# Kernel tuning notes

Hardware: AMD Instinct MI355X
Metric: run time of the kernel (lower is better)

Reference implementation:

```python
import jax, jax.numpy as jnp
import numpy as np

DIM = 3072
NHEADS = 24
HEAD_DIM = DIM // NHEADS  # 128
C = HEAD_DIM // 2         # 64 rotary pairs
B = 2
L = 2048
MAXPOS = 64
EPS = 1e-6
C1 = C - 2 * (C // 3)     # 22 (F band)
C2 = C // 3               # 21 (H band)
C3 = C // 3               # 21 (W band)


def _rope_table():
    # cos/sin table [MAXPOS, C, 2]; three independent frequency bands (F,H,W)
    pos = np.arange(MAXPOS, dtype=np.float32)
    parts = []
    for ck in (C1, C2, C3):
        inv = 1.0 / (10000.0 ** (np.arange(ck, dtype=np.float32) / ck))
        ang = np.outer(pos, inv)
        parts.append(np.stack([np.cos(ang), np.sin(ang)], axis=-1))
    return np.concatenate(parts, axis=1).astype(np.float32)


def setup_inputs() -> dict:
    key = jax.random.key(0)
    ks = jax.random.split(key, 12)
    x = jax.random.normal(ks[0], (B, L, DIM), dtype=jnp.float32)
    grid_sizes = np.array([[4, 16, 28], [4, 16, 32]], dtype=np.int32)  # ragged: 1792, 2048 tokens
    seq_lens = np.array([g[0] * g[1] * g[2] for g in grid_sizes], dtype=np.int32)
    freqs = jnp.asarray(_rope_table())
    w_scale = 0.02
    wq = jax.random.normal(ks[1], (DIM, DIM), dtype=jnp.float32) * w_scale
    wk = jax.random.normal(ks[2], (DIM, DIM), dtype=jnp.float32) * w_scale
    wv = jax.random.normal(ks[3], (DIM, DIM), dtype=jnp.float32) * w_scale
    wo = jax.random.normal(ks[4], (DIM, DIM), dtype=jnp.float32) * w_scale
    bq = jnp.zeros((DIM,), jnp.float32)
    bk = jnp.zeros((DIM,), jnp.float32)
    bv = jnp.zeros((DIM,), jnp.float32)
    bo = jnp.zeros((DIM,), jnp.float32)
    gq = jnp.ones((DIM,), jnp.float32)  # norm_q weight
    gk = jnp.ones((DIM,), jnp.float32)  # norm_k weight
    return {"x": x, "seq_lens": seq_lens, "grid_sizes": grid_sizes, "freqs": freqs,
            "wq": wq, "bq": bq, "wk": wk, "bk": bk, "wv": wv, "bv": bv,
            "wo": wo, "bo": bo, "gq": gq, "gk": gk}


def _rmsnorm(x, g):
    # WanRMSNorm: normalize in bf16, cast back, scale by bf16 weight
    xb = x.astype(jnp.bfloat16)
    n = xb * jax.lax.rsqrt(jnp.mean(xb * xb, axis=-1, keepdims=True) + jnp.bfloat16(EPS))
    return n.astype(x.dtype) * g.astype(jnp.bfloat16)


def _build_rot(grid_sizes, freqs):
    # Per-sample 3D rope rotation table [B, L, C, 2]; padded tail gets identity rotation
    gs = np.asarray(grid_sizes)
    rots = []
    for f, h, w in gs.tolist():
        s = f * h * w
        bf = jnp.broadcast_to(freqs[:f, :C1][:, None, None], (f, h, w, C1, 2))
        bh = jnp.broadcast_to(freqs[:h, C1:C1 + C2][None, :, None], (f, h, w, C2, 2))
        bw = jnp.broadcast_to(freqs[:w, C1 + C2:][None, None, :], (f, h, w, C3, 2))
        rot = jnp.concatenate([bf, bh, bw], axis=3).reshape(s, C, 2)
        if s < L:
            ident = jnp.zeros((L - s, C, 2), freqs.dtype).at[..., 0].set(1.0)
            rot = jnp.concatenate([rot, ident], axis=0)
        rots.append(rot)
    return jnp.stack(rots)


def _apply_rope(x, rot):
    # complex multiply expressed as real rotation; matches rope_apply_3d, output rounded to bf16
    xr = x.reshape(B, L, NHEADS, C, 2)
    cos = rot[:, :, None, :, 0]
    sin = rot[:, :, None, :, 1]
    out_r = xr[..., 0] * cos - xr[..., 1] * sin
    out_i = xr[..., 0] * sin + xr[..., 1] * cos
    out = jnp.stack([out_r, out_i], axis=-1).reshape(B, L, NHEADS, HEAD_DIM)
    return out.astype(jnp.bfloat16).astype(x.dtype)


def reference(x, seq_lens, grid_sizes, freqs, wq, bq, wk, bk, wv, bv, wo, bo, gq, gk):
    q = _rmsnorm(x @ wq + bq, gq).reshape(B, L, NHEADS, HEAD_DIM)
    k = _rmsnorm(x @ wk + bk, gk).reshape(B, L, NHEADS, HEAD_DIM)
    v = (x @ wv + bv).reshape(B, L, NHEADS, HEAD_DIM)
    rot = _build_rot(grid_sizes, freqs)
    q = _apply_rope(q, rot)
    k = _apply_rope(k, rot)
    scale = 1.0 / np.sqrt(HEAD_DIM).astype(np.float32)
    scores = jnp.einsum('bsnd,btnd->bnst', q, k) * scale  # [B, H, L, L]
    kmask = (jnp.arange(L)[None, :] < jnp.asarray(seq_lens)[:, None])[:, None, None, :]
    scores = jnp.where(kmask, scores, jnp.float32(-1e9))
    probs = jax.nn.softmax(scores, axis=-1)
    out = jnp.einsum('bnst,btnd->bsnd', probs, v).reshape(B, L, DIM)
    return out @ wo + bo
```

## Files before the change

kernel.cpp:

```cpp
#include <hip/hip_runtime.h>
#include <stdint.h>
#include <stddef.h>


typedef __attribute__((ext_vector_type(8))) short short8;
typedef __attribute__((ext_vector_type(4))) float f32x4;
typedef __attribute__((ext_vector_type(4))) unsigned short ushort4v;
typedef __attribute__((address_space(1))) uint32_t gu32;
typedef __attribute__((address_space(3))) uint32_t lu32;

__device__ __forceinline__ float btof(unsigned short u){
  union { float f; uint32_t i; } x; x.i = ((uint32_t)u) << 16; return x.f;
}
__device__ __forceinline__ unsigned short ftob(float f){
  uint32_t u = __builtin_bit_cast(uint32_t, f);
  u += 0x7fffu + ((u >> 16) & 1u);
  return (unsigned short)(u >> 16);
}
__device__ __forceinline__ float rb(float f){ return btof(ftob(f)); }

__device__ __forceinline__ void async_cp16(const void* g, void* l){
  __builtin_amdgcn_global_load_lds((gu32*)g, (lu32*)l, 16, 0, 0);
}

__device__ __forceinline__ void barrier_raw(){
  asm volatile("" ::: "memory");
  __builtin_amdgcn_s_barrier();
  asm volatile("" ::: "memory");
}

__device__ __forceinline__ f32x4 vmax4(f32x4 a, f32x4 b){
  f32x4 r;
  r[0] = fmaxf(a[0], b[0]); r[1] = fmaxf(a[1], b[1]);
  r[2] = fmaxf(a[2], b[2]); r[3] = fmaxf(a[3], b[3]);
  return r;
}


__global__ __launch_bounds__(256) void k_convert_x(const float* __restrict__ x,
                                                   unsigned short* __restrict__ xb){
  int i = (blockIdx.x * 256 + threadIdx.x) * 4;
  float4 v = *(const float4*)(x + i);
  ushort4v o = { ftob(v.x), ftob(v.y), ftob(v.z), ftob(v.w) };
  *(ushort4v*)(xb + i) = o;
}

__global__ __launch_bounds__(256) void k_bias(const float* __restrict__ bq,
                                              const float* __restrict__ bk,
                                              const float* __restrict__ bv,
                                              float* __restrict__ bias9){
  int i = blockIdx.x * 256 + threadIdx.x;
  const float* s = (i < 3072) ? bq : ((i < 6144) ? bk : bv);
  bias9[i] = s[i % 3072];
}

__global__ __launch_bounds__(256) void k_wt(const float* __restrict__ wq,
                                            const float* __restrict__ wk,
                                            const float* __restrict__ wv,
                                            const float* __restrict__ wo,
                                            unsigned short* __restrict__ WTqkv,
                                            unsigned short* __restrict__ woT){
  __shared__ float tile[64][65];
  int k0 = blockIdx.x * 64;
  int n0g = blockIdx.y * 64;
  const float* src; unsigned short* dst; int col0, drow0;
  if (n0g < 9216){
    int sel = n0g / 3072;
    src = (sel == 0) ? wq : ((sel == 1) ? wk : wv);
    col0 = n0g % 3072; dst = WTqkv; drow0 = n0g;
  } else { src = wo; col0 = n0g - 9216; dst = woT; drow0 = n0g - 9216; }
  for (int i = 0; i < 16; i++){
    int idx = i * 256 + threadIdx.x;
    int r = idx >> 6, c = idx & 63;
    tile[r][c] = src[(size_t)(k0 + r) * 3072 + col0 + c];
  }
  __syncthreads();
  for (int i = 0; i < 16; i++){
    int idx = i * 256 + threadIdx.x;
    int rr = idx >> 6, cc = idx & 63;
    dst[(size_t)(drow0 + rr) * 3072 + k0 + cc] = ftob(tile[cc][rr]);
  }
}

template <bool OUT_BF16>
__global__ __launch_bounds__(256) void k_gemm(const unsigned short* __restrict__ A,
                                              const unsigned short* __restrict__ BT,
                                              const float* __restrict__ bias,
                                              void* __restrict__ Cout, int N, int K){
  __shared__ __align__(16) unsigned short As[128 * 32];
  __shared__ __align__(16) unsigned short Bs[128 * 32];
  int tid = threadIdx.x;
  int w = tid >> 6, lane = tid & 63;
  int quad = lane >> 4, l16 = lane & 15;
  int m0 = blockIdx.y * 128, n0 = blockIdx.x * 128;
  int wr = w >> 1, wc = w & 1;

  f32x4 acc[4][4] = {};

  int srow = lane >> 2;
  int scol = ((lane & 3) ^ (srow & 3)) * 8;
  const unsigned short* Abase = A + (size_t)(m0 + w * 32 + srow) * K + scol;
  const unsigned short* Bbase = BT + (size_t)(n0 + w * 32 + srow) * K + scol;
  unsigned short* AsW = As + (w * 32) * 32;
  unsigned short* BsW = Bs + (w * 32) * 32;

  for (int kt = 0; kt < K; kt += 32){
    __syncthreads();
    async_cp16(Abase + kt, AsW);
    async_cp16(Abase + kt + (size_t)16 * K, AsW + 16 * 32);
    async_cp16(Bbase + kt, BsW);
    async_cp16(Bbase + kt + (size_t)16 * K, BsW + 16 * 32);
    __syncthreads();
    short8 af[4], bfr[4];
    int csw = (quad ^ (l16 & 3)) * 8;
    for (int im = 0; im < 4; im++)
      af[im] = *(const short8*)(As + (wr * 64 + im * 16 + l16) * 32 + csw);
    for (int in = 0; in < 4; in++)
      bfr[in] = *(const short8*)(Bs + (wc * 64 + in * 16 + l16) * 32 + csw);
    for (int im = 0; im < 4; im++)
      for (int in = 0; in < 4; in++)
        acc[im][in] = __builtin_amdgcn_mfma_f32_16x16x32_bf16(af[im], bfr[in], acc[im][in], 0, 0, 0);
  }

  for (int im = 0; im < 4; im++){
    int row = m0 + wr * 64 + im * 16 + quad * 4;
    for (int in = 0; in < 4; in++){
      int col = n0 + wc * 64 + in * 16 + l16;
      float bb = bias[col];
      f32x4 v = acc[im][in];
      for (int r = 0; r < 4; r++){
        float out = v[r] + bb;
        if (OUT_BF16) ((unsigned short*)Cout)[(size_t)(row + r) * N + col] = ftob(out);
        else          ((float*)Cout)[(size_t)(row + r) * N + col] = out;
      }
    }
  }
}

__global__ __launch_bounds__(256) void k_rmsnorm_rope(const unsigned short* __restrict__ QKVr,
        const float* __restrict__ gq, const float* __restrict__ gk,
        const int* __restrict__ grid_sizes, const float* __restrict__ freqs,
        unsigned short* __restrict__ Qh, unsigned short* __restrict__ Kh){
  int row = blockIdx.x;
  int which = blockIdx.y;
  int b = row >> 11, s = row & 2047;
  const unsigned short* xrow = QKVr + (size_t)row * 9216 + which * 3072;
  const float* g = which ? gk : gq;
  unsigned short* out = which ? Kh : Qh;

  int tid = threadIdx.x, w = tid >> 6, lane = tid & 63;
  float ss = 0.f;
  for (int i = tid * 4; i < 3072; i += 1024){
    ushort4v v = *(const ushort4v*)(xrow + i);
    for (int j = 0; j < 4; j++){
      float f = btof(v[j]);
      ss += btof(ftob(f * f));
    }
  }
  for (int off = 32; off; off >>= 1) ss += __shfl_down(ss, off);
  __shared__ float red[4];
  if (lane == 0) red[w] = ss;
  __syncthreads();
  float tot = red[0] + red[1] + red[2] + red[3];
  float m = rb(tot * (1.0f / 3072.0f));
  m = rb(m + rb(1e-6f));
  float rn = rb(rsqrtf(m));

  int f = grid_sizes[b * 3], hh = grid_sizes[b * 3 + 1], ww = grid_sizes[b * 3 + 2];
  int fhw = f * hh * ww;

  for (int p = tid; p < 1536; p += 256){
    int c = p & 63, hd = p >> 6;
    int e0 = hd * 128 + 2 * c;
    uint32_t xp = *(const uint32_t*)(xrow + e0);
    float2 gg = *(const float2*)(g + e0);
    float x0 = rb(btof((unsigned short)(xp & 0xffffu)) * rn) * rb(gg.x);
    float x1 = rb(btof((unsigned short)(xp >> 16)) * rn) * rb(gg.y);
    float cs = 1.f, sn = 0.f;
    if (s < fhw){
      int pos;
      if (c < 22) pos = s / (hh * ww);
      else if (c < 43) pos = (s / ww) % hh;
      else pos = s % ww;
      float2 f2 = *(const float2*)(freqs + (pos * 64 + c) * 2);
      cs = f2.x; sn = f2.y;
    }
    float o0 = x0 * cs - x1 * sn;
    float o1 = x0 * sn + x1 * cs;
    size_t ob = ((size_t)((b * 24 + hd) * 2048 + s)) * 128 + 2 * c;
    uint32_t op = ((uint32_t)ftob(o1) << 16) | (uint32_t)ftob(o0);
    *(uint32_t*)(out + ob) = op;
  }
}

__global__ __launch_bounds__(256) void k_build_vt(const unsigned short* __restrict__ QKVr,
                                                  unsigned short* __restrict__ Vt){
  __shared__ unsigned short tile[64][132];
  int bh = blockIdx.x;
  int b = bh / 24, h = bh % 24;
  int t0 = blockIdx.y * 64;
  for (int i = 0; i < 8; i++){
    int idx = i * 1024 + threadIdx.x * 4;
    int r = idx >> 7, c = idx & 127;
    *(ushort4v*)&tile[r][c] =
      *(const ushort4v*)&QKVr[(size_t)(b * 2048 + t0 + r) * 9216 + 6144 + h * 128 + c];
  }
  __syncthreads();
  for (int i = 0; i < 8; i++){
    int idx = i * 1024 + threadIdx.x * 4;
    int d = idx >> 6, t = idx & 63;
    ushort4v o4 = { tile[t][d], tile[t + 1][d], tile[t + 2][d], tile[t + 3][d] };
    *(ushort4v*)&Vt[((size_t)bh * 128 + d) * 2048 + t0 + t] = o4;
  }
}

__global__ __launch_bounds__(512, 4) void k_attn(const unsigned short* __restrict__ Q,
              const unsigned short* __restrict__ Kt, const unsigned short* __restrict__ Vt,
              const int* __restrict__ seq_lens, unsigned short* __restrict__ Obuf){
  int qt = blockIdx.x, h = blockIdx.y, b = blockIdx.z;
  int bh = b * 24 + h;
  int tid = threadIdx.x, w = tid >> 6, lane = tid & 63;
  int quad = lane >> 4, l16 = lane & 15;
  int sl = seq_lens[b];
  int nkt = (sl + 63) >> 6;

  __shared__ __align__(16) unsigned short Ks[64 * 128];
  __shared__ __align__(16) unsigned short Vs[128 * 64];
  __shared__ __align__(16) unsigned short Ps[8][16 * 64];

  const unsigned short* Qb = Q + ((size_t)bh * 2048 + qt * 128 + w * 16) * 128;
  short8 qf[4];
  for (int ks = 0; ks < 4; ks++)
    qf[ks] = *(const short8*)(Qb + l16 * 128 + ks * 32 + quad * 8);

  f32x4 o[8] = {};
  float mrow = -1e30f, lrow = 0.f;

  const float ksc = 0.08838834764831845f * 1.4426950408889634f;

  const unsigned short* Kg0 = Kt + (size_t)bh * 2048 * 128;
  const unsigned short* Vg0 = Vt + (size_t)bh * 128 * 2048;

  int vrow = lane >> 3;
  int vchunk = (lane & 7) ^ (vrow & 7);

  auto stageK = [&](int t0){
    for (int i = 0; i < 2; i++){
      int rowi = w * 8 + i * 4;
      int kchunk = l16 ^ ((rowi + quad) & 15);
      async_cp16(Kg0 + (size_t)(t0 + rowi + quad) * 128 + kchunk * 8,
                 (unsigned short*)Ks + rowi * 128);
    }
  };
  auto stageV = [&](int t0){
    for (int i = 0; i < 2; i++){
      int rowi = w * 16 + i * 8;
      async_cp16(Vg0 + (size_t)(rowi + vrow) * 2048 + t0 + vchunk * 8,
                 (unsigned short*)Vs + rowi * 64);
    }
  };

  stageK(0);
  asm volatile("s_waitcnt vmcnt(0)" ::: "memory");
  barrier_raw();

  for (int kt = 0; kt < nkt; kt++){
    int t0 = kt * 64;

    stageV(t0);

    f32x4 sac[4] = {};
    for (int ks = 0; ks < 4; ks++){
      int kcs = ((ks * 4 + quad) ^ l16) * 8;
      short8 kf[4];
      for (int ct = 0; ct < 4; ct++)
        kf[ct] = *(const short8*)(Ks + (ct * 16 + l16) * 128 + kcs);
      __builtin_amdgcn_s_setprio(1);
      for (int ct = 0; ct < 4; ct++)
        sac[ct] = __builtin_amdgcn_mfma_f32_16x16x32_bf16(kf[ct], qf[ks], sac[ct], 0, 0, 0);
      __builtin_amdgcn_s_setprio(0);
    }

    asm volatile("s_waitcnt lgkmcnt(0)" ::: "memory");
    barrier_raw();

    bool haveK = (kt + 1 < nkt);
    if (haveK) stageK(t0 + 64);

    if (t0 + 64 > sl){
      for (int ct = 0; ct < 4; ct++)
        for (int r = 0; r < 4; r++)
          if (t0 + ct * 16 + quad * 4 + r >= sl) sac[ct][r] = -1e30f;
    }

    {
      f32x4 m03 = vmax4(vmax4(sac[0], sac[1]), vmax4(sac[2], sac[3]));
      float mx = fmaxf(fmaxf(m03[0], m03[1]), fmaxf(m03[2], m03[3]));
      mx = fmaxf(mx, __shfl_xor(mx, 16));
      mx = fmaxf(mx, __shfl_xor(mx, 32));
      float mnew = mrow;
      if (!__all((mx - mrow) * ksc <= 11.5f)){
        mnew = fmaxf(mrow, mx);
        float alpha = exp2f((mrow - mnew) * ksc);
        mrow = mnew;
        lrow *= alpha;
        for (int r = 0; r < 4; r++){
          float ar = __shfl(alpha, quad * 4 + r, 16);
          for (int dt = 0; dt < 8; dt++) o[dt][r] *= ar;
        }
      }
      float psum = 0.f;
      for (int ct = 0; ct < 4; ct++){
        ushort4v pw;
        for (int r = 0; r < 4; r++){
          float p = exp2f((sac[ct][r] - mnew) * ksc);
          unsigned short pb = ftob(p);
          psum += btof(pb);
          pw[r] = pb;
        }
        int cpos = (ct * 2 + (quad >> 1)) ^ (l16 & 7);
        *(ushort4v*)&Ps[w][l16 * 64 + cpos * 8 + (quad & 1) * 4] = pw;
      }
      psum += __shfl_xor(psum, 16);
      psum += __shfl_xor(psum, 32);
      lrow += psum;
    }

    if (haveK) asm volatile("s_waitcnt vmcnt(2)" ::: "memory");
    else       asm volatile("s_waitcnt vmcnt(0)" ::: "memory");
    barrier_raw();

    asm volatile("s_waitcnt lgkmcnt(0)" ::: "memory");

    for (int ks = 0; ks < 2; ks++){
      int vcs = ((ks * 4 + quad) ^ (l16 & 7)) * 8;
      short8 pf = *(const short8*)(&Ps[w][l16 * 64 + vcs]);
      for (int dh = 0; dh < 2; dh++){
        short8 vf[4];
        for (int dt = 0; dt < 4; dt++)
          vf[dt] = *(const short8*)(Vs + ((dh * 4 + dt) * 16 + l16) * 64 + vcs);
        __builtin_amdgcn_s_setprio(1);
        for (int dt = 0; dt < 4; dt++)
          o[dh * 4 + dt] = __builtin_amdgcn_mfma_f32_16x16x32_bf16(pf, vf[dt], o[dh * 4 + dt], 0, 0, 0);
        __builtin_amdgcn_s_setprio(0);
      }
    }

    asm volatile("s_waitcnt lgkmcnt(0)" ::: "memory");
    asm volatile("s_waitcnt vmcnt(0)" ::: "memory");
    barrier_raw();
  }

  float inv = 1.0f / lrow;
  for (int r = 0; r < 4; r++){
    float invr = __shfl(inv, quad * 4 + r, 16);
    int s = qt * 128 + w * 16 + quad * 4 + r;
    size_t base = (size_t)(b * 2048 + s) * 3072 + h * 128;
    for (int dt = 0; dt < 8; dt++)
      Obuf[base + dt * 16 + l16] = ftob(o[dt][r] * invr);
  }
}


extern "C" void kernel_launch(void* const* d_in, const int* in_sizes, int n_in,
                              void* d_out, int out_size, void* d_ws, size_t ws_size,
                              hipStream_t stream){
  const float* x          = (const float*)d_in[0];
  const int*   seq_lens   = (const int*)d_in[1];
  const int*   grid_sizes = (const int*)d_in[2];
  const float* freqs      = (const float*)d_in[3];
  const float* wq = (const float*)d_in[4];
  const float* bq = (const float*)d_in[5];
  const float* wk = (const float*)d_in[6];
  const float* bk = (const float*)d_in[7];
  const float* wv = (const float*)d_in[8];
  const float* bv = (const float*)d_in[9];
  const float* wo = (const float*)d_in[10];
  const float* bo = (const float*)d_in[11];
  const float* gq = (const float*)d_in[12];
  const float* gk = (const float*)d_in[13];

  char* ws = (char*)d_ws;
  unsigned short* Xb    = (unsigned short*)(ws);
  unsigned short* WTqkv = (unsigned short*)(ws + 25165824);
  unsigned short* woT   = (unsigned short*)(ws + 81788928);
  float*          bias9 = (float*)(ws + 100663296);
  unsigned short* QKVr  = (unsigned short*)(ws + 100700160);
  unsigned short* Qh    = (unsigned short*)(ws + 176197632);
  unsigned short* Kh    = (unsigned short*)(ws + 201363456);
  unsigned short* Vth   = (unsigned short*)(ws + 226529280);
  unsigned short* Obuf  = Xb;

  k_convert_x<<<12288, 256, 0, stream>>>(x, Xb);
  k_bias<<<36, 256, 0, stream>>>(bq, bk, bv, bias9);
  k_wt<<<dim3(48, 192), 256, 0, stream>>>(wq, wk, wv, wo, WTqkv, woT);
  k_gemm<true><<<dim3(72, 32), 256, 0, stream>>>(Xb, WTqkv, bias9, QKVr, 9216, 3072);
  k_rmsnorm_rope<<<dim3(4096, 2), 256, 0, stream>>>(QKVr, gq, gk, grid_sizes, freqs, Qh, Kh);
  k_build_vt<<<dim3(48, 32), 256, 0, stream>>>(QKVr, Vth);
  k_attn<<<dim3(16, 24, 2), 512, 0, stream>>>(Qh, Kh, Vth, seq_lens, Obuf);
  k_gemm<false><<<dim3(24, 32), 256, 0, stream>>>(Obuf, woT, bo, (float*)d_out, 3072, 3072);
}
```

Measured before the change: 821.5 us.

## Double-buffer GEMM LDS tiles with async prefetch and XCD-aware block swizzle

The GEMM kernel now keeps two LDS buffers and issues the global-to-LDS copies for the next K-tile before computing on the current one, using explicit vmcnt waits and raw barriers in place of two __syncthreads per iteration. The LDS layout is changed to 128-element rows with an XOR swizzle meant to avoid bank conflicts on fragment reads. Workgroup indices are remapped so that consecutive tiles land on the same XCD, which should improve L2 reuse. LDS use doubles, and the correctness of the manual waitcnt counts depends on each thread issuing exactly four async copies per stage.

```diff
diff --git a/kernel.cpp b/kernel.cpp
--- a/kernel.cpp
+++ b/kernel.cpp
@@ -87,39 +87,69 @@
                                               const unsigned short* __restrict__ BT,
                                               const float* __restrict__ bias,
                                               void* __restrict__ Cout, int N, int K){
-  __shared__ __align__(16) unsigned short As[128 * 32];
-  __shared__ __align__(16) unsigned short Bs[128 * 32];
+  __shared__ __align__(16) unsigned short As[2][32 * 128];
+  __shared__ __align__(16) unsigned short Bs[2][32 * 128];
   int tid = threadIdx.x;
   int w = tid >> 6, lane = tid & 63;
   int quad = lane >> 4, l16 = lane & 15;
-  int m0 = blockIdx.y * 128, n0 = blockIdx.x * 128;
   int wr = w >> 1, wc = w & 1;
 
+  int nwg = gridDim.x * gridDim.y;
+  int flat = blockIdx.y * gridDim.x + blockIdx.x;
+  int cpx = nwg >> 3;
+  int swz = (flat & 7) * cpx + (flat >> 3);
+  int n0 = (swz % gridDim.x) * 128;
+  int m0 = (swz / gridDim.x) * 128;
+
   f32x4 acc[4][4] = {};
 
-  int srow = lane >> 2;
-  int scol = ((lane & 3) ^ (srow & 3)) * 8;
-  const unsigned short* Abase = A + (size_t)(m0 + w * 32 + srow) * K + scol;
-  const unsigned short* Bbase = BT + (size_t)(n0 + w * 32 + srow) * K + scol;
-  unsigned short* AsW = As + (w * 32) * 32;
-  unsigned short* BsW = Bs + (w * 32) * 32;
-
-  for (int kt = 0; kt < K; kt += 32){
-    __syncthreads();
-    async_cp16(Abase + kt, AsW);
-    async_cp16(Abase + kt + (size_t)16 * K, AsW + 16 * 32);
-    async_cp16(Bbase + kt, BsW);
-    async_cp16(Bbase + kt + (size_t)16 * K, BsW + 16 * 32);
-    __syncthreads();
+  int sj = lane >> 4, sc = lane & 15;
+
+  auto stage = [&](int buf, int kt){
+    for (int i = 0; i < 2; i++){
+      int rowb = w * 8 + i * 4;
+      int j = rowb + sj;
+      int lc = sc ^ (j & 15);
+      int sub = lc >> 2, kc = lc & 3;
+      async_cp16(A + (size_t)(m0 + j * 4 + sub) * K + kt + kc * 8,
+                 (unsigned short*)&As[buf][rowb * 128]);
+      async_cp16(BT + (size_t)(n0 + j * 4 + sub) * K + kt + kc * 8,
+                 (unsigned short*)&Bs[buf][rowb * 128]);
+    }
+  };
+
+  int nt = K >> 5;
+  stage(0, 0);
+
+  for (int t = 0; t < nt; t++){
+    int cur = t & 1;
+    if (t + 1 < nt){
+      stage(cur ^ 1, (t + 1) << 5);
+      asm volatile("s_waitcnt vmcnt(4)" ::: "memory");
+    } else {
+      asm volatile("s_waitcnt vmcnt(0)" ::: "memory");
+    }
+    barrier_raw();
+
+    const unsigned short* Ab = &As[cur][0];
+    const unsigned short* Bb = &Bs[cur][0];
     short8 af[4], bfr[4];
-    int csw = (quad ^ (l16 & 3)) * 8;
-    for (int im = 0; im < 4; im++)
-      af[im] = *(const short8*)(As + (wr * 64 + im * 16 + l16) * 32 + csw);
-    for (int in = 0; in < 4; in++)
-      bfr[in] = *(const short8*)(Bs + (wc * 64 + in * 16 + l16) * 32 + csw);
+    for (int im = 0; im < 4; im++){
+      int j = wr * 16 + im * 4 + (l16 >> 2);
+      int phys = ((l16 & 3) * 4 + quad) ^ (j & 15);
+      af[im] = *(const short8*)(Ab + j * 128 + phys * 8);
+    }
+    for (int in = 0; in < 4; in++){
+      int j = wc * 16 + in * 4 + (l16 >> 2);
+      int phys = ((l16 & 3) * 4 + quad) ^ (j & 15);
+      bfr[in] = *(const short8*)(Bb + j * 128 + phys * 8);
+    }
     for (int im = 0; im < 4; im++)
       for (int in = 0; in < 4; in++)
         acc[im][in] = __builtin_amdgcn_mfma_f32_16x16x32_bf16(af[im], bfr[in], acc[im][in], 0, 0, 0);
+
+    asm volatile("s_waitcnt lgkmcnt(0)" ::: "memory");
+    barrier_raw();
   }
 
   for (int im = 0; im < 4; im++){
```

Result: no change. 813.7 us (-1.0%).

## Rewrite GEMM as 256x256 double-buffered tile with staged async loads

Applied to the files above, without the earlier changes.

Replaces the 128x128 single-buffered bf16 MFMA GEMM with a 256x256 tile over 512 threads, K-step 64, double-buffered in 128KB of dynamic LDS. Loads for the next K tile are issued in four quarters, interleaved with MFMA quarters and ordered by explicit vmcnt waits. It also uses an XOR-swizzled LDS layout and raises MFMA issue priority. The aim is to hide global-load latency and raise data reuse for the QKV and output projections. The cost is more barriers, high register pressure, and fewer blocks for the smaller output GEMM (192 blocks), which may underfill the GPU.

```diff
diff --git a/kernel.cpp b/kernel.cpp
--- a/kernel.cpp
+++ b/kernel.cpp
@@ -35,6 +35,10 @@
   r[2] = fmaxf(a[2], b[2]); r[3] = fmaxf(a[3], b[3]);
   return r;
 }
+
+#define VMW4 asm volatile("s_waitcnt vmcnt(4)" ::: "memory")
+#define VMW2 asm volatile("s_waitcnt vmcnt(2)" ::: "memory")
+#define VMW0 asm volatile("s_waitcnt vmcnt(0)" ::: "memory")
 
 
 __global__ __launch_bounds__(256) void k_convert_x(const float* __restrict__ x,
@@ -83,51 +87,127 @@
 }
 
 template <bool OUT_BF16>
-__global__ __launch_bounds__(256) void k_gemm(const unsigned short* __restrict__ A,
-                                              const unsigned short* __restrict__ BT,
-                                              const float* __restrict__ bias,
-                                              void* __restrict__ Cout, int N, int K){
-  __shared__ __align__(16) unsigned short As[128 * 32];
-  __shared__ __align__(16) unsigned short Bs[128 * 32];
+__global__ __launch_bounds__(512, 2) void k_gemm(const unsigned short* __restrict__ A,
+                                                 const unsigned short* __restrict__ BT,
+                                                 const float* __restrict__ bias,
+                                                 void* __restrict__ Cout, int N, int K){
+  extern __shared__ unsigned short lds[];
+  unsigned short* AsL = lds;
+  unsigned short* BsL = lds + 32768;
+
   int tid = threadIdx.x;
   int w = tid >> 6, lane = tid & 63;
   int quad = lane >> 4, l16 = lane & 15;
-  int m0 = blockIdx.y * 128, n0 = blockIdx.x * 128;
-  int wr = w >> 1, wc = w & 1;
-
-  f32x4 acc[4][4] = {};
-
-  int srow = lane >> 2;
-  int scol = ((lane & 3) ^ (srow & 3)) * 8;
-  const unsigned short* Abase = A + (size_t)(m0 + w * 32 + srow) * K + scol;
-  const unsigned short* Bbase = BT + (size_t)(n0 + w * 32 + srow) * K + scol;
-  unsigned short* AsW = As + (w * 32) * 32;
-  unsigned short* BsW = Bs + (w * 32) * 32;
-
-  for (int kt = 0; kt < K; kt += 32){
-    __syncthreads();
-    async_cp16(Abase + kt, AsW);
-    async_cp16(Abase + kt + (size_t)16 * K, AsW + 16 * 32);
-    async_cp16(Bbase + kt, BsW);
-    async_cp16(Bbase + kt + (size_t)16 * K, BsW + 16 * 32);
-    __syncthreads();
-    short8 af[4], bfr[4];
-    int csw = (quad ^ (l16 & 3)) * 8;
+  int wr = w >> 2, wc = w & 3;
+  int m0 = blockIdx.y * 256, n0 = blockIdx.x * 256;
+
+  f32x4 acc[8][4] = {};
+  short8 af[4][2], b0[2][2], b1[2][2];
+
+  auto lda = [&](const unsigned short* base, int mh){
+#pragma unroll
     for (int im = 0; im < 4; im++)
-      af[im] = *(const short8*)(As + (wr * 64 + im * 16 + l16) * 32 + csw);
-    for (int in = 0; in < 4; in++)
-      bfr[in] = *(const short8*)(Bs + (wc * 64 + in * 16 + l16) * 32 + csw);
+#pragma unroll
+      for (int kk = 0; kk < 2; kk++){
+        int j = wr * 64 + mh * 32 + im * 8 + (l16 >> 1);
+        int lc = ((l16 & 1) << 3) | (kk << 2) | quad;
+        af[im][kk] = *(const short8*)(base + j * 128 + (lc ^ (j & 15)) * 8);
+      }
+  };
+  auto ldb = [&](const unsigned short* base, short8 (&bb)[2][2], int nh){
+#pragma unroll
+    for (int in = 0; in < 2; in++)
+#pragma unroll
+      for (int kk = 0; kk < 2; kk++){
+        int j = wc * 32 + nh * 16 + in * 8 + (l16 >> 1);
+        int lc = ((l16 & 1) << 3) | (kk << 2) | quad;
+        bb[in][kk] = *(const short8*)(base + j * 128 + (lc ^ (j & 15)) * 8);
+      }
+  };
+  auto mfmaQ = [&](int mh, short8 (&bb)[2][2], int nh){
+    __builtin_amdgcn_s_setprio(1);
+#pragma unroll
     for (int im = 0; im < 4; im++)
-      for (int in = 0; in < 4; in++)
-        acc[im][in] = __builtin_amdgcn_mfma_f32_16x16x32_bf16(af[im], bfr[in], acc[im][in], 0, 0, 0);
-  }
-
-  for (int im = 0; im < 4; im++){
-    int row = m0 + wr * 64 + im * 16 + quad * 4;
-    for (int in = 0; in < 4; in++){
-      int col = n0 + wc * 64 + in * 16 + l16;
+#pragma unroll
+      for (int in = 0; in < 2; in++)
+#pragma unroll
+        for (int kk = 0; kk < 2; kk++)
+          acc[mh * 4 + im][nh * 2 + in] =
+            __builtin_amdgcn_mfma_f32_16x16x32_bf16(af[im][kk], bb[in][kk],
+                                                    acc[mh * 4 + im][nh * 2 + in], 0, 0, 0);
+    __builtin_amdgcn_s_setprio(0);
+  };
+
+  auto stageA = [&](unsigned short* dst, int kt, int mh){
+#pragma unroll
+    for (int i = 0; i < 2; i++){
+      int idx0 = (w * 2 + i) * 8;
+      int mr0 = (((idx0 >> 6) << 7) | (idx0 & 63)) | (mh << 6);
+      int jb = mr0 >> 1;
+      int j = jb + (lane >> 4);
+      int lc = (lane & 15) ^ (j & 15);
+      int mr = (j << 1) + (lc >> 3);
+      async_cp16(A + (size_t)(m0 + mr) * K + kt + (lc & 7) * 8, dst + jb * 128);
+    }
+  };
+  auto stageB = [&](unsigned short* dst, int kt, int nh){
+#pragma unroll
+    for (int i = 0; i < 2; i++){
+      int idx0 = (w * 2 + i) * 8;
+      int nr0 = (((idx0 >> 5) << 6) | (idx0 & 31)) | (nh << 5);
+      int jb = nr0 >> 1;
+      int j = jb + (lane >> 4);
+      int lc = (lane & 15) ^ (j & 15);
+      int nr = (j << 1) + (lc >> 3);
+      async_cp16(BT + (size_t)(n0 + nr) * K + kt + (lc & 7) * 8, dst + jb * 128);
+    }
+  };
+
+  int nt = K >> 6;
+  stageA(AsL, 0, 0); stageB(BsL, 0, 0); stageB(BsL, 0, 1); stageA(AsL, 0, 1);
+  VMW4; barrier_raw();
+
+  for (int t = 0; t < nt; t++){
+    unsigned short* Asb = AsL + (t & 1) * 16384;
+    unsigned short* Bsb = BsL + (t & 1) * 16384;
+    unsigned short* Asn = AsL + ((t & 1) ^ 1) * 16384;
+    unsigned short* Bsn = BsL + ((t & 1) ^ 1) * 16384;
+    int ktn = (t + 1) << 6;
+    bool more = (t + 1 < nt);
+
+    lda(Asb, 0); ldb(Bsb, b0, 0);
+    if (more) stageA(Asn, ktn, 0);
+    VMW4; barrier_raw();
+    mfmaQ(0, b0, 0);
+    barrier_raw();
+
+    ldb(Bsb, b1, 1);
+    if (more){ stageB(Bsn, ktn, 0); VMW4; } else VMW2;
+    barrier_raw();
+    mfmaQ(0, b1, 1);
+    barrier_raw();
+
+    lda(Asb, 1);
+    if (more){ stageB(Bsn, ktn, 1); VMW4; } else VMW0;
+    barrier_raw();
+    mfmaQ(1, b1, 1);
+    barrier_raw();
+
+    if (more){ stageA(Asn, ktn, 1); VMW4; }
+    barrier_raw();
+    mfmaQ(1, b0, 0);
+    barrier_raw();
+  }
+
+#pragma unroll
+  for (int img = 0; img < 8; img++){
+    int row = m0 + wr * 128 + img * 16 + quad * 4;
+#pragma unroll
+    for (int ing = 0; ing < 4; ing++){
+      int col = n0 + wc * 64 + ing * 16 + l16;
       float bb = bias[col];
-      f32x4 v = acc[im][in];
+      f32x4 v = acc[img][ing];
+#pragma unroll
       for (int r = 0; r < 4; r++){
         float out = v[r] + bb;
         if (OUT_BF16) ((unsigned short*)Cout)[(size_t)(row + r) * N + col] = ftob(out);
@@ -391,12 +471,21 @@
   unsigned short* Vth   = (unsigned short*)(ws + 226529280);
   unsigned short* Obuf  = Xb;
 
+  static bool s_attr = false;
+  if (!s_attr){
+    hipFuncSetAttribute(reinterpret_cast<const void*>(&k_gemm<true>),
+                        hipFuncAttributeMaxDynamicSharedMemorySize, 131072);
+    hipFuncSetAttribute(reinterpret_cast<const void*>(&k_gemm<false>),
+                        hipFuncAttributeMaxDynamicSharedMemorySize, 131072);
+    s_attr = true;
+  }
+
   k_convert_x<<<12288, 256, 0, stream>>>(x, Xb);
   k_bias<<<36, 256, 0, stream>>>(bq, bk, bv, bias9);
   k_wt<<<dim3(48, 192), 256, 0, stream>>>(wq, wk, wv, wo, WTqkv, woT);
-  k_gemm<true><<<dim3(72, 32), 256, 0, stream>>>(Xb, WTqkv, bias9, QKVr, 9216, 3072);
+  k_gemm<true><<<dim3(36, 16), 512, 131072, stream>>>(Xb, WTqkv, bias9, QKVr, 9216, 3072);
   k_rmsnorm_rope<<<dim3(4096, 2), 256, 0, stream>>>(QKVr, gq, gk, grid_sizes, freqs, Qh, Kh);
   k_build_vt<<<dim3(48, 32), 256, 0, stream>>>(QKVr, Vth);
   k_attn<<<dim3(16, 24, 2), 512, 0, stream>>>(Qh, Kh, Vth, seq_lens, Obuf);
-  k_gemm<false><<<dim3(24, 32), 256, 0, stream>>>(Obuf, woT, bo, (float*)d_out, 3072, 3072);
-}
+  k_gemm<false><<<dim3(12, 16), 512, 131072, stream>>>(Obuf, woT, bo, (float*)d_out, 3072, 3072);
+}
```

After: 748.3 us, median of 2. 8.9% less time.
